# Kernel optimization log

Hardware: AMD Instinct MI355X
Metric: run time of the kernel (lower is better)

The kernel has to match this reference:

```python
import jax, jax.numpy as jnp
import numpy as np

BETA = 0.9
THRESHOLD = 0.9
SIM_TIME = 100

@jax.custom_vjp
def spike(u):
    # snntorch ATan surrogate spike: forward heaviside, backward 1/(1+(pi*u)^2) (alpha=2)
    return (u > 0).astype(u.dtype)

def _spike_fwd(u):
    return (u > 0).astype(u.dtype), u

def _spike_bwd(u, g):
    return (g / (1.0 + (jnp.pi * u) ** 2),)

spike.defvjp(_spike_fwd, _spike_bwd)

def setup_inputs() -> dict:
    key = jax.random.key(0)
    k1, k2, k3 = jax.random.split(key, 3)
    B, D, H = 2048, 1024, 256
    x = jax.random.normal(k1, (B, D), dtype=jnp.float32)
    enc_w = jax.random.normal(k2, (D, H), dtype=jnp.float32) * 0.1
    dec_w = jax.random.normal(k3, (H, D), dtype=jnp.float32) * 0.1
    return {"x": x, "enc_w": enc_w, "dec_w": dec_w}

def _snn_forward(x, enc_w, dec_w):
    B = x.shape[0]
    D, H = enc_w.shape
    dt = x.dtype
    # input current is constant across timesteps (x fixed); hoist the matmul
    in_cur = x @ enc_w  # [B, H]

    def step(carry, _):
        # NOTE: original repo swaps snntorch's (spk, mem) return, so the
        # carried "mem" state is actually the previous spike train, and the
        # membrane potential is what flows into the decoder matmul.
        s_e, s_d, _, _ = carry
        reset_e = jax.lax.stop_gradient((s_e > THRESHOLD).astype(dt))
        m_e = BETA * s_e + in_cur - reset_e * THRESHOLD          # [B, H]
        spk_e = spike(m_e - THRESHOLD)
        out_cur = m_e @ dec_w                                    # [B, D] (mem used as 'spikes')
        reset_d = jax.lax.stop_gradient((s_d > THRESHOLD).astype(dt))
        m_d = BETA * s_d + out_cur - reset_d * THRESHOLD         # [B, D]
        spk_d = spike(m_d - THRESHOLD)
        return (spk_e, spk_d, m_e, m_d), None

    init = (jnp.zeros((B, H), dt), jnp.zeros((B, D), dt),
            jnp.zeros((B, H), dt), jnp.zeros((B, D), dt))
    (s_e, s_d, m_e, m_d), _ = jax.lax.scan(step, init, None, length=SIM_TIME)
    # original returns (spikes_decoder, spikes_encoder) which hold the membranes
    return m_d, m_e

def reference(x, enc_w, dec_w):
    return _snn_forward(x, enc_w, dec_w)
```

## Files before the change

### kernel.cpp

```cpp
#include <hip/hip_runtime.h>


typedef __attribute__((ext_vector_type(8))) short bf16x8;
typedef __attribute__((ext_vector_type(4))) float f32x4;
typedef __attribute__((ext_vector_type(8))) unsigned short ushort8;

__device__ __forceinline__ unsigned short f2bf(float f) {
    unsigned u = __builtin_bit_cast(unsigned, f);
    unsigned r = u + 0x7FFFu + ((u >> 16) & 1u);
    return (unsigned short)(r >> 16);
}

template <int ROWS>
__device__ __forceinline__ void stage_tile(const unsigned short* __restrict__ g,
                                           int ld, unsigned short* lds, int t) {
    #pragma unroll
    for (int c = 0; c < ROWS / 32; ++c) {
        const int idx = c * 256 + t;
        const int row = idx >> 3;
        const int chunk = (idx & 7) ^ (row & 7);
        const unsigned short* src = g + (size_t)row * ld + chunk * 8;
        unsigned short* dst = lds + (size_t)(idx & ~63) * 8;
        __builtin_amdgcn_global_load_lds(
            (const __attribute__((address_space(1))) void*)src,
            (__attribute__((address_space(3))) void*)dst, 16, 0, 0);
    }
}

template <int BM, int BN, bool WBF>
__global__ __launch_bounds__(256) void mfma_gemm(
    const unsigned short* __restrict__ A,
    const unsigned short* __restrict__ B,
    float* __restrict__ C,
    unsigned short* __restrict__ Cbf,
    int M, int N, int K)
{
    constexpr int BK = 64;
    constexpr int WM = BM / 2, WN = BN / 2;
    constexpr int FM = WM / 16, FN = WN / 16;
    __shared__ __align__(16) unsigned short As[2][BM * BK];
    __shared__ __align__(16) unsigned short Bs[2][BN * BK];

    const int t = threadIdx.x;
    const int lane = t & 63;
    const int l15 = lane & 15, l4 = lane >> 4;
    const int wid = t >> 6;
    const int wr = wid >> 1, wc = wid & 1;
    const int brow = blockIdx.y * BM, bcol = blockIdx.x * BN;

    f32x4 acc[FM][FN];
    #pragma unroll
    for (int i = 0; i < FM; ++i)
        #pragma unroll
        for (int j = 0; j < FN; ++j) acc[i][j] = {0.f, 0.f, 0.f, 0.f};

    const unsigned short* Ab = A + (size_t)brow * K;
    const unsigned short* Bb = B + (size_t)bcol * K;
    const int NT = K / BK;

    stage_tile<BM>(Ab, K, As[0], t);
    stage_tile<BN>(Bb, K, Bs[0], t);
    int cur = 0;
    for (int kt = 0; kt < NT; ++kt) {
        __syncthreads();
        if (kt + 1 < NT) {
            stage_tile<BM>(Ab + (kt + 1) * BK, K, As[cur ^ 1], t);
            stage_tile<BN>(Bb + (kt + 1) * BK, K, Bs[cur ^ 1], t);
        }
        #pragma unroll
        for (int s = 0; s < 2; ++s) {
            bf16x8 aF[FM], bF[FN];
            #pragma unroll
            for (int i = 0; i < FM; ++i) {
                const int r = wr * WM + i * 16 + l15;
                const int ch = (s * 4 + l4) ^ (r & 7);
                aF[i] = *(const bf16x8*)&As[cur][r * BK + ch * 8];
            }
            #pragma unroll
            for (int j = 0; j < FN; ++j) {
                const int r = wc * WN + j * 16 + l15;
                const int ch = (s * 4 + l4) ^ (r & 7);
                bF[j] = *(const bf16x8*)&Bs[cur][r * BK + ch * 8];
            }
            #pragma unroll
            for (int i = 0; i < FM; ++i)
                #pragma unroll
                for (int j = 0; j < FN; ++j)
                    acc[i][j] = __builtin_amdgcn_mfma_f32_16x16x32_bf16(
                        aF[i], bF[j], acc[i][j], 0, 0, 0);
        }
        cur ^= 1;
    }

    #pragma unroll
    for (int i = 0; i < FM; ++i)
        #pragma unroll
        for (int j = 0; j < FN; ++j)
            #pragma unroll
            for (int reg = 0; reg < 4; ++reg) {
                const int row = brow + wr * WM + i * 16 + l4 * 4 + reg;
                const int col = bcol + wc * WN + j * 16 + l15;
                const float v = acc[i][j][reg];
                C[(size_t)row * N + col] = v;
                if (WBF) Cbf[(size_t)row * N + col] = f2bf(v);
            }
}

__global__ __launch_bounds__(256) void gemm2_kres(
    const unsigned short* __restrict__ A,
    const unsigned short* __restrict__ B,
    float* __restrict__ C)
{
    constexpr int K = 256, N = 1024;
    __shared__ __align__(16) unsigned short As[4][32 * 64];
    __shared__ __align__(16) unsigned short Bs[4][64 * 64];

    const int t = threadIdx.x;
    const int lane = t & 63;
    const int l15 = lane & 15, l4 = lane >> 4;
    const int wid = t >> 6;
    const int wr = wid >> 1, wc = wid & 1;
    const int brow = blockIdx.y * 32, bcol = blockIdx.x * 64;

    #pragma unroll
    for (int kt = 0; kt < 4; ++kt) {
        stage_tile<32>(A + (size_t)brow * K + kt * 64, K, As[kt], t);
        stage_tile<64>(B + (size_t)bcol * K + kt * 64, K, Bs[kt], t);
    }
    __syncthreads();

    f32x4 acc[2] = {{0.f, 0.f, 0.f, 0.f}, {0.f, 0.f, 0.f, 0.f}};
    #pragma unroll
    for (int kt = 0; kt < 4; ++kt)
        #pragma unroll
        for (int s = 0; s < 2; ++s) {
            const int ra = wr * 16 + l15;
            const int cha = (s * 4 + l4) ^ (ra & 7);
            bf16x8 aF = *(const bf16x8*)&As[kt][ra * 64 + cha * 8];
            #pragma unroll
            for (int j = 0; j < 2; ++j) {
                const int rb = wc * 32 + j * 16 + l15;
                const int chb = (s * 4 + l4) ^ (rb & 7);
                bf16x8 bF = *(const bf16x8*)&Bs[kt][rb * 64 + chb * 8];
                acc[j] = __builtin_amdgcn_mfma_f32_16x16x32_bf16(aF, bF, acc[j], 0, 0, 0);
            }
        }

    #pragma unroll
    for (int j = 0; j < 2; ++j)
        #pragma unroll
        for (int reg = 0; reg < 4; ++reg) {
            const int row = brow + wr * 16 + l4 * 4 + reg;
            const int col = bcol + wc * 32 + j * 16 + l15;
            C[(size_t)row * N + col] = acc[j][reg];
        }
}

__global__ __launch_bounds__(256) void prep(
    const float* __restrict__ x, const float* __restrict__ enc,
    const float* __restrict__ dec, unsigned short* __restrict__ x_bf,
    unsigned short* __restrict__ encT, unsigned short* __restrict__ decT)
{
    __shared__ unsigned short tile[32][33];
    const int bid = blockIdx.x;
    const int t = threadIdx.x;

    if (bid < 1024) {
        const int i = bid * 256 + t;
        float4 a = ((const float4*)x)[2 * i];
        float4 b = ((const float4*)x)[2 * i + 1];
        ushort8 v;
        v[0] = f2bf(a.x); v[1] = f2bf(a.y); v[2] = f2bf(a.z); v[3] = f2bf(a.w);
        v[4] = f2bf(b.x); v[5] = f2bf(b.y); v[6] = f2bf(b.z); v[7] = f2bf(b.w);
        ((ushort8*)x_bf)[i] = v;
        return;
    }
    const float* in; unsigned short* out; int R, C, bx, by;
    if (bid < 1280) {
        const int bb = bid - 1024;
        in = enc; out = encT; R = 1024; C = 256; bx = bb % 8; by = bb / 8;
    } else {
        const int bb = bid - 1280;
        in = dec; out = decT; R = 256; C = 1024; bx = bb % 32; by = bb / 32;
    }
    const int r0 = by * 32, c0 = bx * 32;
    const int tx = t % 32, ty = t / 32;
    #pragma unroll
    for (int k = 0; k < 4; ++k) {
        const int lr = ty + k * 8;
        tile[lr][tx] = f2bf(in[(size_t)(r0 + lr) * C + c0 + tx]);
    }
    __syncthreads();
    #pragma unroll
    for (int k = 0; k < 4; ++k) {
        const int lc = ty + k * 8;
        out[(size_t)(c0 + lc) * R + r0 + tx] = tile[tx][lc];
    }
}

#define BKF 32
#define PADF 4
template <int BM, int BN, int TM, int TN>
__global__ __launch_bounds__(256) void gemm_f32(
    const float* __restrict__ A, const float* __restrict__ B,
    float* __restrict__ C, int M, int N, int K)
{
    __shared__ float As[BKF][BM + PADF];
    __shared__ float Bs[BKF][BN + PADF];
    const int t = threadIdx.x;
    const int brow = blockIdx.y * BM, bcol = blockIdx.x * BN;
    constexpr int NTX = BN / TN;
    const int tx = t % NTX, ty = t / NTX;
    float acc[TM][TN];
    #pragma unroll
    for (int i = 0; i < TM; ++i)
        #pragma unroll
        for (int j = 0; j < TN; ++j) acc[i][j] = 0.f;
    for (int k0 = 0; k0 < K; k0 += BKF) {
        #pragma unroll
        for (int v = t; v < BM * BKF / 4; v += 256) {
            const int row = v / (BKF / 4), kv = v % (BKF / 4);
            const float4 val = *(const float4*)&A[(size_t)(brow + row) * K + k0 + kv * 4];
            As[kv * 4 + 0][row] = val.x; As[kv * 4 + 1][row] = val.y;
            As[kv * 4 + 2][row] = val.z; As[kv * 4 + 3][row] = val.w;
        }
        #pragma unroll
        for (int v = t; v < BKF * BN / 4; v += 256) {
            const int kk = v / (BN / 4), cv = v % (BN / 4);
            *(float4*)&Bs[kk][cv * 4] = *(const float4*)&B[(size_t)(k0 + kk) * N + bcol + cv * 4];
        }
        __syncthreads();
        #pragma unroll
        for (int k = 0; k < BKF; ++k) {
            float a[TM], b[TN];
            #pragma unroll
            for (int i = 0; i < TM; ++i) a[i] = As[k][ty * TM + i];
            #pragma unroll
            for (int j = 0; j < TN; ++j) b[j] = Bs[k][tx * TN + j];
            #pragma unroll
            for (int i = 0; i < TM; ++i)
                #pragma unroll
                for (int j = 0; j < TN; ++j) acc[i][j] = fmaf(a[i], b[j], acc[i][j]);
        }
        __syncthreads();
    }
    #pragma unroll
    for (int i = 0; i < TM; ++i)
        #pragma unroll
        for (int j = 0; j < TN; ++j)
            C[(size_t)(brow + ty * TM + i) * N + bcol + tx * TN + j] = acc[i][j];
}

extern "C" void kernel_launch(void* const* d_in, const int* in_sizes, int n_in,
                              void* d_out, int out_size, void* d_ws, size_t ws_size,
                              hipStream_t stream) {
    const float* x     = (const float*)d_in[0];
    const float* enc_w = (const float*)d_in[1];
    const float* dec_w = (const float*)d_in[2];

    const int B = 2048, D = 1024, H = 256;
    float* m_d = (float*)d_out;
    float* m_e = (float*)d_out + (size_t)B * D;

    const size_t need = (size_t)B * D * 2 + (size_t)D * H * 2
                      + (size_t)H * D * 2 + (size_t)B * H * 2;
    if (ws_size >= need) {
        unsigned short* x_bf  = (unsigned short*)d_ws;
        unsigned short* encT  = x_bf + (size_t)B * D;
        unsigned short* decT  = encT + (size_t)H * D;
        unsigned short* me_bf = decT + (size_t)D * H;

        prep<<<dim3(1536), dim3(256), 0, stream>>>(x, enc_w, dec_w, x_bf, encT, decT);

        mfma_gemm<32, 32, true><<<dim3(H / 32, B / 32), dim3(256), 0, stream>>>(
            x_bf, encT, m_e, me_bf, B, H, D);
        gemm2_kres<<<dim3(D / 64, B / 32), dim3(256), 0, stream>>>(me_bf, decT, m_d);
    } else {
        gemm_f32<64, 32, 4, 2><<<dim3(H / 32, B / 64), dim3(256), 0, stream>>>(x, enc_w, m_e, B, H, D);
        gemm_f32<64, 64, 4, 4><<<dim3(D / 64, B / 64), dim3(256), 0, stream>>>(m_e, dec_w, m_d, B, D, H);
    }
}
```

Measured before the change: 26.36 us.

## Fuse x bf16 conversion into GEMM1 and add triple-buffered LDS pipeline

Drops the separate pass that converts x to bf16. The first GEMM now stages fp32 x tiles straight into LDS through a swizzled global_load_lds and converts them to bf16 in registers before the MFMA. The K loop also moves from double to triple buffering with explicit vmcnt waits and raw barriers, so two tiles are in flight while one is computed. This removes the write and re-read of a 4 MB bf16 copy of x, but GEMM1 now reads fp32 data, twice the bytes, from each of its 8 column blocks and spends more LDS and ALU time per tile.

```diff
diff --git a/kernel.cpp b/kernel.cpp
--- a/kernel.cpp
+++ b/kernel.cpp
@@ -27,83 +27,89 @@
     }
 }
 
-template <int BM, int BN, bool WBF>
-__global__ __launch_bounds__(256) void mfma_gemm(
-    const unsigned short* __restrict__ A,
-    const unsigned short* __restrict__ B,
+template <int ROWS>
+__device__ __forceinline__ void stage_tile_f32(const float* __restrict__ g,
+                                               int ld, float* lds, int t) {
+    #pragma unroll
+    for (int c = 0; c < ROWS / 16; ++c) {
+        const int idx = c * 256 + t;
+        const int row = idx >> 4;
+        const int chunk = (idx & 15) ^ (row & 15);
+        const float* src = g + (size_t)row * ld + chunk * 4;
+        float* dst = lds + (size_t)(idx & ~63) * 4;
+        __builtin_amdgcn_global_load_lds(
+            (const __attribute__((address_space(1))) void*)src,
+            (__attribute__((address_space(3))) void*)dst, 16, 0, 0);
+    }
+}
+
+__global__ __launch_bounds__(256) void gemm1_pipe(
+    const float* __restrict__ x,
+    const unsigned short* __restrict__ Bt,
     float* __restrict__ C,
-    unsigned short* __restrict__ Cbf,
-    int M, int N, int K)
-{
-    constexpr int BK = 64;
-    constexpr int WM = BM / 2, WN = BN / 2;
-    constexpr int FM = WM / 16, FN = WN / 16;
-    __shared__ __align__(16) unsigned short As[2][BM * BK];
-    __shared__ __align__(16) unsigned short Bs[2][BN * BK];
+    unsigned short* __restrict__ Cbf)
+{
+    constexpr int N = 256, K = 1024, BK = 64, NT = K / BK;
+    __shared__ __align__(16) float          As[3][32 * 64];
+    __shared__ __align__(16) unsigned short Bs[3][32 * 64];
 
     const int t = threadIdx.x;
     const int lane = t & 63;
     const int l15 = lane & 15, l4 = lane >> 4;
     const int wid = t >> 6;
     const int wr = wid >> 1, wc = wid & 1;
-    const int brow = blockIdx.y * BM, bcol = blockIdx.x * BN;
-
-    f32x4 acc[FM][FN];
-    #pragma unroll
-    for (int i = 0; i < FM; ++i)
-        #pragma unroll
-        for (int j = 0; j < FN; ++j) acc[i][j] = {0.f, 0.f, 0.f, 0.f};
-
-    const unsigned short* Ab = A + (size_t)brow * K;
-    const unsigned short* Bb = B + (size_t)bcol * K;
-    const int NT = K / BK;
-
-    stage_tile<BM>(Ab, K, As[0], t);
-    stage_tile<BN>(Bb, K, Bs[0], t);
-    int cur = 0;
+    const int brow = blockIdx.y * 32, bcol = blockIdx.x * 32;
+
+    const float* Ab = x + (size_t)brow * K;
+    const unsigned short* Bb = Bt + (size_t)bcol * K;
+
+    f32x4 acc = {0.f, 0.f, 0.f, 0.f};
+
+    stage_tile_f32<32>(Ab, K, As[0], t);
+    stage_tile<32>(Bb, K, Bs[0], t);
+    stage_tile_f32<32>(Ab + BK, K, As[1], t);
+    stage_tile<32>(Bb + BK, K, Bs[1], t);
+
     for (int kt = 0; kt < NT; ++kt) {
-        __syncthreads();
-        if (kt + 1 < NT) {
-            stage_tile<BM>(Ab + (kt + 1) * BK, K, As[cur ^ 1], t);
-            stage_tile<BN>(Bb + (kt + 1) * BK, K, Bs[cur ^ 1], t);
-        }
+        if (kt + 1 < NT) { asm volatile("s_waitcnt vmcnt(3)" ::: "memory"); }
+        else             { asm volatile("s_waitcnt vmcnt(0)" ::: "memory"); }
+        __builtin_amdgcn_s_barrier();
+        __builtin_amdgcn_sched_barrier(0);
+
+        if (kt + 2 < NT) {
+            const int nb = (kt + 2) % 3;
+            stage_tile_f32<32>(Ab + (kt + 2) * BK, K, As[nb], t);
+            stage_tile<32>(Bb + (kt + 2) * BK, K, Bs[nb], t);
+        }
+
+        const int cur = kt % 3;
+        const int ra = wr * 16 + l15;
+        const int rb = wc * 16 + l15;
         #pragma unroll
         for (int s = 0; s < 2; ++s) {
-            bf16x8 aF[FM], bF[FN];
-            #pragma unroll
-            for (int i = 0; i < FM; ++i) {
-                const int r = wr * WM + i * 16 + l15;
-                const int ch = (s * 4 + l4) ^ (r & 7);
-                aF[i] = *(const bf16x8*)&As[cur][r * BK + ch * 8];
-            }
-            #pragma unroll
-            for (int j = 0; j < FN; ++j) {
-                const int r = wc * WN + j * 16 + l15;
-                const int ch = (s * 4 + l4) ^ (r & 7);
-                bF[j] = *(const bf16x8*)&Bs[cur][r * BK + ch * 8];
-            }
-            #pragma unroll
-            for (int i = 0; i < FM; ++i)
-                #pragma unroll
-                for (int j = 0; j < FN; ++j)
-                    acc[i][j] = __builtin_amdgcn_mfma_f32_16x16x32_bf16(
-                        aF[i], bF[j], acc[i][j], 0, 0, 0);
-        }
-        cur ^= 1;
-    }
-
-    #pragma unroll
-    for (int i = 0; i < FM; ++i)
-        #pragma unroll
-        for (int j = 0; j < FN; ++j)
-            #pragma unroll
-            for (int reg = 0; reg < 4; ++reg) {
-                const int row = brow + wr * WM + i * 16 + l4 * 4 + reg;
-                const int col = bcol + wc * WN + j * 16 + l15;
-                const float v = acc[i][j][reg];
-                C[(size_t)row * N + col] = v;
-                if (WBF) Cbf[(size_t)row * N + col] = f2bf(v);
-            }
+            const int c0 = (s * 8 + l4 * 2) ^ l15;
+            const int c1 = (s * 8 + l4 * 2 + 1) ^ l15;
+            const f32x4 a0 = *(const f32x4*)&As[cur][ra * 64 + c0 * 4];
+            const f32x4 a1 = *(const f32x4*)&As[cur][ra * 64 + c1 * 4];
+            bf16x8 aF;
+            aF[0] = (short)f2bf(a0[0]); aF[1] = (short)f2bf(a0[1]);
+            aF[2] = (short)f2bf(a0[2]); aF[3] = (short)f2bf(a0[3]);
+            aF[4] = (short)f2bf(a1[0]); aF[5] = (short)f2bf(a1[1]);
+            aF[6] = (short)f2bf(a1[2]); aF[7] = (short)f2bf(a1[3]);
+            const int cb = (s * 4 + l4) ^ (rb & 7);
+            const bf16x8 bF = *(const bf16x8*)&Bs[cur][rb * 64 + cb * 8];
+            acc = __builtin_amdgcn_mfma_f32_16x16x32_bf16(aF, bF, acc, 0, 0, 0);
+        }
+    }
+
+    #pragma unroll
+    for (int reg = 0; reg < 4; ++reg) {
+        const int row = brow + wr * 16 + l4 * 4 + reg;
+        const int col = bcol + wc * 16 + l15;
+        const float v = acc[reg];
+        C[(size_t)row * N + col] = v;
+        Cbf[(size_t)row * N + col] = f2bf(v);
+    }
 }
 
 __global__ __launch_bounds__(256) void gemm2_kres(
@@ -156,31 +162,19 @@
         }
 }
 
-__global__ __launch_bounds__(256) void prep(
-    const float* __restrict__ x, const float* __restrict__ enc,
-    const float* __restrict__ dec, unsigned short* __restrict__ x_bf,
+__global__ __launch_bounds__(256) void prep_t(
+    const float* __restrict__ enc, const float* __restrict__ dec,
     unsigned short* __restrict__ encT, unsigned short* __restrict__ decT)
 {
     __shared__ unsigned short tile[32][33];
     const int bid = blockIdx.x;
     const int t = threadIdx.x;
 
-    if (bid < 1024) {
-        const int i = bid * 256 + t;
-        float4 a = ((const float4*)x)[2 * i];
-        float4 b = ((const float4*)x)[2 * i + 1];
-        ushort8 v;
-        v[0] = f2bf(a.x); v[1] = f2bf(a.y); v[2] = f2bf(a.z); v[3] = f2bf(a.w);
-        v[4] = f2bf(b.x); v[5] = f2bf(b.y); v[6] = f2bf(b.z); v[7] = f2bf(b.w);
-        ((ushort8*)x_bf)[i] = v;
-        return;
-    }
     const float* in; unsigned short* out; int R, C, bx, by;
-    if (bid < 1280) {
-        const int bb = bid - 1024;
-        in = enc; out = encT; R = 1024; C = 256; bx = bb % 8; by = bb / 8;
+    if (bid < 256) {
+        in = enc; out = encT; R = 1024; C = 256; bx = bid % 8; by = bid / 8;
     } else {
-        const int bb = bid - 1280;
+        const int bb = bid - 256;
         in = dec; out = decT; R = 256; C = 1024; bx = bb % 32; by = bb / 32;
     }
     const int r0 = by * 32, c0 = bx * 32;
@@ -262,18 +256,15 @@
     float* m_d = (float*)d_out;
     float* m_e = (float*)d_out + (size_t)B * D;
 
-    const size_t need = (size_t)B * D * 2 + (size_t)D * H * 2
-                      + (size_t)H * D * 2 + (size_t)B * H * 2;
+    const size_t need = (size_t)D * H * 2 * 2 + (size_t)B * H * 2;
     if (ws_size >= need) {
-        unsigned short* x_bf  = (unsigned short*)d_ws;
-        unsigned short* encT  = x_bf + (size_t)B * D;
+        unsigned short* encT  = (unsigned short*)d_ws;
         unsigned short* decT  = encT + (size_t)H * D;
         unsigned short* me_bf = decT + (size_t)D * H;
 
-        prep<<<dim3(1536), dim3(256), 0, stream>>>(x, enc_w, dec_w, x_bf, encT, decT);
-
-        mfma_gemm<32, 32, true><<<dim3(H / 32, B / 32), dim3(256), 0, stream>>>(
-            x_bf, encT, m_e, me_bf, B, H, D);
+        prep_t<<<dim3(512), dim3(256), 0, stream>>>(enc_w, dec_w, encT, decT);
+
+        gemm1_pipe<<<dim3(H / 32, B / 32), dim3(256), 0, stream>>>(x, encT, m_e, me_bf);
         gemm2_kres<<<dim3(D / 64, B / 32), dim3(256), 0, stream>>>(me_bf, decT, m_d);
     } else {
         gemm_f32<64, 32, 4, 2><<<dim3(H / 32, B / 64), dim3(256), 0, stream>>>(x, enc_w, m_e, B, H, D);
```

Measured after the change: 28.52 us. 8.2% more time.

## Fuse encoder and decoder GEMMs into one kernel keeping m_e tile in LDS

Applied to the files above, without the earlier changes.

Replaces the two GEMM launches with one fused kernel. Each 512-thread block computes a 32-row slice of m_e across all 256 columns, converts it to bf16 in LDS, and then streams decT in 64-column chunks to produce m_d. This removes the global bf16 round trip of m_e and one kernel launch. The cost is a grid of only 64 blocks on a GPU with many more CUs, so occupancy and parallelism drop sharply, and every block re-reads all of encT and decT.

```diff
diff --git a/kernel.cpp b/kernel.cpp
--- a/kernel.cpp
+++ b/kernel.cpp
@@ -11,149 +11,130 @@
     return (unsigned short)(r >> 16);
 }
 
-template <int ROWS>
-__device__ __forceinline__ void stage_tile(const unsigned short* __restrict__ g,
-                                           int ld, unsigned short* lds, int t) {
-    #pragma unroll
-    for (int c = 0; c < ROWS / 32; ++c) {
-        const int idx = c * 256 + t;
-        const int row = idx >> 3;
-        const int chunk = (idx & 7) ^ (row & 7);
-        const unsigned short* src = g + (size_t)row * ld + chunk * 8;
-        unsigned short* dst = lds + (size_t)(idx & ~63) * 8;
-        __builtin_amdgcn_global_load_lds(
-            (const __attribute__((address_space(1))) void*)src,
-            (__attribute__((address_space(3))) void*)dst, 16, 0, 0);
-    }
-}
-
-template <int BM, int BN, bool WBF>
-__global__ __launch_bounds__(256) void mfma_gemm(
-    const unsigned short* __restrict__ A,
-    const unsigned short* __restrict__ B,
-    float* __restrict__ C,
-    unsigned short* __restrict__ Cbf,
-    int M, int N, int K)
+__device__ __forceinline__ void gload_lds16(const unsigned short* src,
+                                            unsigned short* dst) {
+    __builtin_amdgcn_global_load_lds(
+        (const __attribute__((address_space(1))) void*)src,
+        (__attribute__((address_space(3))) void*)dst, 16, 0, 0);
+}
+
+__global__ __launch_bounds__(512) void fused_gemm(
+    const unsigned short* __restrict__ x_bf,
+    const unsigned short* __restrict__ encT,
+    const unsigned short* __restrict__ decT,
+    float* __restrict__ m_e,
+    float* __restrict__ m_d)
 {
-    constexpr int BK = 64;
-    constexpr int WM = BM / 2, WN = BN / 2;
-    constexpr int FM = WM / 16, FN = WN / 16;
-    __shared__ __align__(16) unsigned short As[2][BM * BK];
-    __shared__ __align__(16) unsigned short Bs[2][BN * BK];
+    constexpr int K1 = 1024, N1 = 256, K2 = 256, N2 = 1024, BM = 32, BK = 64;
+    __shared__ __align__(16) unsigned short sm_me[BM * 256];
+    __shared__ __align__(16) unsigned short sm_big[2][BM * BK + 256 * BK];
 
     const int t = threadIdx.x;
     const int lane = t & 63;
     const int l15 = lane & 15, l4 = lane >> 4;
     const int wid = t >> 6;
-    const int wr = wid >> 1, wc = wid & 1;
-    const int brow = blockIdx.y * BM, bcol = blockIdx.x * BN;
-
-    f32x4 acc[FM][FN];
-    #pragma unroll
-    for (int i = 0; i < FM; ++i)
-        #pragma unroll
-        for (int j = 0; j < FN; ++j) acc[i][j] = {0.f, 0.f, 0.f, 0.f};
-
-    const unsigned short* Ab = A + (size_t)brow * K;
-    const unsigned short* Bb = B + (size_t)bcol * K;
-    const int NT = K / BK;
-
-    stage_tile<BM>(Ab, K, As[0], t);
-    stage_tile<BN>(Bb, K, Bs[0], t);
-    int cur = 0;
-    for (int kt = 0; kt < NT; ++kt) {
-        __syncthreads();
-        if (kt + 1 < NT) {
-            stage_tile<BM>(Ab + (kt + 1) * BK, K, As[cur ^ 1], t);
-            stage_tile<BN>(Bb + (kt + 1) * BK, K, Bs[cur ^ 1], t);
-        }
+    const int wr = wid >> 2;
+    const int wc = wid & 3;
+    const int brow = blockIdx.x * BM;
+
+    f32x4 acc[4];
+    #pragma unroll
+    for (int j = 0; j < 4; ++j) acc[j] = {0.f, 0.f, 0.f, 0.f};
+
+    auto stageA = [&](int kt, unsigned short* buf) {
+        if (t < 256) {
+            const int row = t >> 3, cc = t & 7;
+            const unsigned short* src =
+                x_bf + (size_t)(brow + row) * K1 + kt * BK + (cc ^ (row & 7)) * 8;
+            gload_lds16(src, buf + (size_t)(t & ~63) * 8);
+        }
+        unsigned short* bbuf = buf + BM * BK;
+        #pragma unroll
+        for (int c = 0; c < 4; ++c) {
+            const int idx = c * 512 + t;
+            const int row = idx >> 3, cc = idx & 7;
+            const unsigned short* src =
+                encT + (size_t)row * K1 + kt * BK + (cc ^ (row & 7)) * 8;
+            gload_lds16(src, bbuf + (size_t)(idx & ~63) * 8);
+        }
+    };
+
+    stageA(0, sm_big[0]);
+    for (int kt = 0; kt < K1 / BK; ++kt) {
+        __syncthreads();
+        if (kt + 1 < K1 / BK) stageA(kt + 1, sm_big[(kt + 1) & 1]);
+        const unsigned short* As = sm_big[kt & 1];
+        const unsigned short* Bs = As + BM * BK;
+        const int ra = wr * 16 + l15;
         #pragma unroll
         for (int s = 0; s < 2; ++s) {
-            bf16x8 aF[FM], bF[FN];
-            #pragma unroll
-            for (int i = 0; i < FM; ++i) {
-                const int r = wr * WM + i * 16 + l15;
-                const int ch = (s * 4 + l4) ^ (r & 7);
-                aF[i] = *(const bf16x8*)&As[cur][r * BK + ch * 8];
-            }
-            #pragma unroll
-            for (int j = 0; j < FN; ++j) {
-                const int r = wc * WN + j * 16 + l15;
-                const int ch = (s * 4 + l4) ^ (r & 7);
-                bF[j] = *(const bf16x8*)&Bs[cur][r * BK + ch * 8];
-            }
-            #pragma unroll
-            for (int i = 0; i < FM; ++i)
-                #pragma unroll
-                for (int j = 0; j < FN; ++j)
-                    acc[i][j] = __builtin_amdgcn_mfma_f32_16x16x32_bf16(
-                        aF[i], bF[j], acc[i][j], 0, 0, 0);
-        }
-        cur ^= 1;
-    }
-
-    #pragma unroll
-    for (int i = 0; i < FM; ++i)
-        #pragma unroll
-        for (int j = 0; j < FN; ++j)
-            #pragma unroll
-            for (int reg = 0; reg < 4; ++reg) {
-                const int row = brow + wr * WM + i * 16 + l4 * 4 + reg;
-                const int col = bcol + wc * WN + j * 16 + l15;
-                const float v = acc[i][j][reg];
-                C[(size_t)row * N + col] = v;
-                if (WBF) Cbf[(size_t)row * N + col] = f2bf(v);
-            }
-}
-
-__global__ __launch_bounds__(256) void gemm2_kres(
-    const unsigned short* __restrict__ A,
-    const unsigned short* __restrict__ B,
-    float* __restrict__ C)
-{
-    constexpr int K = 256, N = 1024;
-    __shared__ __align__(16) unsigned short As[4][32 * 64];
-    __shared__ __align__(16) unsigned short Bs[4][64 * 64];
-
-    const int t = threadIdx.x;
-    const int lane = t & 63;
-    const int l15 = lane & 15, l4 = lane >> 4;
-    const int wid = t >> 6;
-    const int wr = wid >> 1, wc = wid & 1;
-    const int brow = blockIdx.y * 32, bcol = blockIdx.x * 64;
-
-    #pragma unroll
-    for (int kt = 0; kt < 4; ++kt) {
-        stage_tile<32>(A + (size_t)brow * K + kt * 64, K, As[kt], t);
-        stage_tile<64>(B + (size_t)bcol * K + kt * 64, K, Bs[kt], t);
-    }
-    __syncthreads();
-
-    f32x4 acc[2] = {{0.f, 0.f, 0.f, 0.f}, {0.f, 0.f, 0.f, 0.f}};
-    #pragma unroll
-    for (int kt = 0; kt < 4; ++kt)
-        #pragma unroll
-        for (int s = 0; s < 2; ++s) {
-            const int ra = wr * 16 + l15;
-            const int cha = (s * 4 + l4) ^ (ra & 7);
-            bf16x8 aF = *(const bf16x8*)&As[kt][ra * 64 + cha * 8];
-            #pragma unroll
-            for (int j = 0; j < 2; ++j) {
-                const int rb = wc * 32 + j * 16 + l15;
-                const int chb = (s * 4 + l4) ^ (rb & 7);
-                bf16x8 bF = *(const bf16x8*)&Bs[kt][rb * 64 + chb * 8];
+            const int ca = (s * 4 + l4) ^ (ra & 7);
+            const bf16x8 aF = *(const bf16x8*)&As[ra * BK + ca * 8];
+            #pragma unroll
+            for (int j = 0; j < 4; ++j) {
+                const int rb = wc * 64 + j * 16 + l15;
+                const int cb = (s * 4 + l4) ^ (rb & 7);
+                const bf16x8 bF = *(const bf16x8*)&Bs[rb * BK + cb * 8];
                 acc[j] = __builtin_amdgcn_mfma_f32_16x16x32_bf16(aF, bF, acc[j], 0, 0, 0);
             }
         }
-
-    #pragma unroll
-    for (int j = 0; j < 2; ++j)
+    }
+
+    #pragma unroll
+    for (int j = 0; j < 4; ++j)
+        #pragma unroll
+        for (int reg = 0; reg < 4; ++reg) {
+            const int r = wr * 16 + l4 * 4 + reg;
+            const int ccol = wc * 64 + j * 16 + l15;
+            const float v = acc[j][reg];
+            m_e[(size_t)(brow + r) * N1 + ccol] = v;
+            const int cc = (ccol >> 3) ^ (r & 7);
+            sm_me[r * 256 + cc * 8 + (ccol & 7)] = f2bf(v);
+        }
+
+    __syncthreads();
+
+    bf16x8 aF2[8];
+    {
+        const int ra = wr * 16 + l15;
+        #pragma unroll
+        for (int ks = 0; ks < 8; ++ks) {
+            const int ca = (ks * 4 + l4) ^ (ra & 7);
+            aF2[ks] = *(const bf16x8*)&sm_me[ra * 256 + ca * 8];
+        }
+    }
+
+    auto stageD = [&](int nc, unsigned short* buf) {
+        #pragma unroll
+        for (int c = 0; c < 4; ++c) {
+            const int idx = c * 512 + t;
+            const int row = idx >> 5, cc = idx & 31;
+            const unsigned short* src =
+                decT + (size_t)(nc * 64 + row) * K2 + (cc ^ (row & 7)) * 8;
+            gload_lds16(src, buf + (size_t)(idx & ~63) * 8);
+        }
+    };
+
+    stageD(0, sm_big[0]);
+    for (int nc = 0; nc < 16; ++nc) {
+        __syncthreads();
+        if (nc + 1 < 16) stageD(nc + 1, sm_big[(nc + 1) & 1]);
+        const unsigned short* Ds = sm_big[nc & 1];
+        f32x4 acc2 = {0.f, 0.f, 0.f, 0.f};
+        const int rb = wc * 16 + l15;
+        #pragma unroll
+        for (int ks = 0; ks < 8; ++ks) {
+            const int cb = (ks * 4 + l4) ^ (rb & 7);
+            const bf16x8 bF = *(const bf16x8*)&Ds[rb * K2 + cb * 8];
+            acc2 = __builtin_amdgcn_mfma_f32_16x16x32_bf16(aF2[ks], bF, acc2, 0, 0, 0);
+        }
         #pragma unroll
         for (int reg = 0; reg < 4; ++reg) {
             const int row = brow + wr * 16 + l4 * 4 + reg;
-            const int col = bcol + wc * 32 + j * 16 + l15;
-            C[(size_t)row * N + col] = acc[j][reg];
-        }
+            const int col = nc * 64 + wc * 16 + l15;
+            m_d[(size_t)row * N2 + col] = acc2[reg];
+        }
+    }
 }
 
 __global__ __launch_bounds__(256) void prep(
@@ -262,19 +243,14 @@
     float* m_d = (float*)d_out;
     float* m_e = (float*)d_out + (size_t)B * D;
 
-    const size_t need = (size_t)B * D * 2 + (size_t)D * H * 2
-                      + (size_t)H * D * 2 + (size_t)B * H * 2;
+    const size_t need = (size_t)B * D * 2 + (size_t)D * H * 2 * 2;
     if (ws_size >= need) {
-        unsigned short* x_bf  = (unsigned short*)d_ws;
-        unsigned short* encT  = x_bf + (size_t)B * D;
-        unsigned short* decT  = encT + (size_t)H * D;
-        unsigned short* me_bf = decT + (size_t)D * H;
+        unsigned short* x_bf = (unsigned short*)d_ws;
+        unsigned short* encT = x_bf + (size_t)B * D;
+        unsigned short* decT = encT + (size_t)H * D;
 
         prep<<<dim3(1536), dim3(256), 0, stream>>>(x, enc_w, dec_w, x_bf, encT, decT);
-
-        mfma_gemm<32, 32, true><<<dim3(H / 32, B / 32), dim3(256), 0, stream>>>(
-            x_bf, encT, m_e, me_bf, B, H, D);
-        gemm2_kres<<<dim3(D / 64, B / 32), dim3(256), 0, stream>>>(me_bf, decT, m_d);
+        fused_gemm<<<dim3(B / 32), dim3(512), 0, stream>>>(x_bf, encT, decT, m_e, m_d);
     } else {
         gemm_f32<64, 32, 4, 2><<<dim3(H / 32, B / 64), dim3(256), 0, stream>>>(x, enc_w, m_e, B, H, D);
         gemm_f32<64, 64, 4, 4><<<dim3(D / 64, B / 64), dim3(256), 0, stream>>>(m_e, dec_w, m_d, B, D, H);
```

After: 34.23 us. +29.9%, slower.
